# Kernel optimization log

Measured on AMD Instinct MI355X. Metric: run time of the kernel, lower is better.

Reference implementation:

```python
import jax, jax.numpy as jnp
import numpy as np
import math

WINDOW_LEFT = 512   # sliding-window: each query attends to keys in [q-512, q]
WINDOW_RIGHT = 0    # causal
NEG_INF = -1e30


def setup_inputs() -> dict:
    key = jax.random.key(0)
    kq, kk, kv, ks = jax.random.split(key, 4)
    B, S, H, D = 2, 2048, 16, 128
    q = jax.random.normal(kq, (B, S, H, D), dtype=jnp.float32)
    k = jax.random.normal(kk, (B, S, H, D), dtype=jnp.float32)
    v = jax.random.normal(kv, (B, S, H, D), dtype=jnp.float32)
    # geometric-ish ALiBi slopes per head (positive, decaying), like flash-attn
    alibi_slopes = jax.random.uniform(ks, (H,), dtype=jnp.float32, minval=0.001, maxval=0.5)
    return {"q": q, "k": k, "v": v, "alibi_slopes": alibi_slopes}


def reference(q, k, v, alibi_slopes):
    # q,k,v: [B, S, H, D]; alibi_slopes: [H]
    B, S, H, D = q.shape
    scale = 1.0 / math.sqrt(D)
    # scores: [B, H, Sq, Sk]
    scores = jnp.einsum("bqhd,bkhd->bhqk", q, k) * scale
    qi = jnp.arange(S)[:, None]
    ki = jnp.arange(S)[None, :]
    rel = ki - qi  # [Sq, Sk], <=0 for past keys
    # ALiBi bias (equal q/k lengths): -slope * |q - k|
    alibi = -alibi_slopes[:, None, None] * jnp.abs(rel).astype(scores.dtype)  # [H,Sq,Sk]
    scores = scores + alibi[None, :, :, :]
    # causal + sliding-window mask: allow WINDOW_RIGHT future, WINDOW_LEFT past
    mask = (rel <= WINDOW_RIGHT) & (rel >= -WINDOW_LEFT)  # [Sq, Sk]
    scores = jnp.where(mask[None, None, :, :], scores, NEG_INF)
    p = jax.nn.softmax(scores, axis=-1)
    out = jnp.einsum("bhqk,bkhd->bqhd", p, v)
    return out
```

## Files before the change

### kernel.cpp

```cpp
#include <hip/hip_runtime.h>
#include <hip/hip_bf16.h>

typedef __attribute__((ext_vector_type(8))) __bf16 bf16x8;
typedef __attribute__((ext_vector_type(2))) __bf16 bf16x2;
typedef __attribute__((ext_vector_type(4))) float f32x4;

#define MFMA32(a, b, c) __builtin_amdgcn_mfma_f32_16x16x32_bf16((a), (b), (c), 0, 0, 0)

constexpr int Bc = 2, Sc = 2048, Hc = 16, Dc = 128;
constexpr int HD = Hc * Dc;
constexpr int QB = 256;
constexpr float SCALE_L2 = (float)(0.08838834764831844 * 1.4426950408889634);
constexpr float LOG2E = 1.4426950408889634f;
constexpr float NEGF = -30000.0f;
constexpr int KSTR = 2080;

__device__ inline bf16x8 cvt8(f32x4 a, f32x4 b) {
    bf16x8 r;
    r[0]=(__bf16)a[0]; r[1]=(__bf16)a[1]; r[2]=(__bf16)a[2]; r[3]=(__bf16)a[3];
    r[4]=(__bf16)b[0]; r[5]=(__bf16)b[1]; r[6]=(__bf16)b[2]; r[7]=(__bf16)b[3];
    return r;
}

__global__ __launch_bounds__(512, 2) void lumen_attn_kernel(
    const float* __restrict__ Q, const float* __restrict__ K,
    const float* __restrict__ V, const float* __restrict__ SLP,
    float* __restrict__ O)
{
    __shared__ __align__(16) char k_lds[2][64 * 256];
    __shared__ __align__(16) char v_lds[2][8 * KSTR];

    const int tid  = threadIdx.x;
    const int lane = tid & 63;
    const int wid  = tid >> 6;
    const int cl = lane & 15;
    const int kg = lane >> 4;

    const int bid = blockIdx.x;
    const int swz = (bid & 7) * 32 + (bid >> 3);
    const int qb  = (swz & 7) * QB;
    const int bh  = swz >> 3;
    const int h = bh & 15, b = bh >> 4;

    const float slope = SLP[h] * LOG2E;
    const size_t base = (size_t)b * Sc * HD + (size_t)h * Dc;
    const float* qp = Q + base;
    const float* kp = K + base;
    const float* vp = V + base;
    float*       op = O + base;

    const int qw = qb + wid * 32;

    bf16x8 qf[2][4];
    #pragma unroll
    for (int s = 0; s < 2; ++s) {
        const float* qrow = qp + (size_t)(qw + s * 16 + cl) * HD + kg * 8;
        #pragma unroll
        for (int c = 0; c < 4; ++c) {
            f32x4 a = *(const f32x4*)(qrow + c * 32);
            f32x4 bq = *(const f32x4*)(qrow + c * 32 + 4);
            #pragma unroll
            for (int i = 0; i < 4; ++i) { a[i] *= SCALE_L2; bq[i] *= SCALE_L2; }
            qf[s][c] = cvt8(a, bq);
        }
    }

    f32x4 o_acc[2][8];
    #pragma unroll
    for (int s = 0; s < 2; ++s)
        #pragma unroll
        for (int nn = 0; nn < 8; ++nn) o_acc[s][nn] = f32x4{0.f, 0.f, 0.f, 0.f};
    float ssum[2] = {0.f, 0.f};

    int voff[8];
    #pragma unroll
    for (int nn = 0; nn < 8; ++nn) {
        const int d = nn * 16 + cl;
        const int s = (d & ~7) | ((d & 7) ^ ((d >> 3) & 7));
        voff[nn] = s * 16;
    }

    const int kb0    = qb > 512 ? qb - 512 : 0;
    const int kb_end = qb + QB - 64;
    const int NT     = (kb_end - kb0) / 64 + 1;

    const int ktk = tid >> 3;
    const int kd0 = (tid & 7) * 16;
    const int kpos = (2 * ((ktk >> 5) & 1) + ((ktk >> 2) & 1)) * 16
                   + ((ktk >> 3) & 3) * 4 + (ktk & 3);
    const int ksw = (kpos & 15) << 4;
    const int vtk = tid >> 4;
    const int vd0 = (tid & 15) * 8;
    const int va_ = tid & 15;

    f32x4 ra, rb, rc, rd, sa, sb, sc, sd;

    #define LOAD(kbn) do {                                                     \
        const float* kr_ = kp + (size_t)((kbn) + ktk) * HD + kd0;              \
        ra = *(const f32x4*)kr_;        rb = *(const f32x4*)(kr_ + 4);         \
        rc = *(const f32x4*)(kr_ + 8);  rd = *(const f32x4*)(kr_ + 12);        \
        const float* vr_ = vp + (size_t)((kbn) + 2 * vtk) * HD + vd0;          \
        sa = *(const f32x4*)vr_;        sb = *(const f32x4*)(vr_ + 4);         \
        sc = *(const f32x4*)(vr_ + HD); sd = *(const f32x4*)(vr_ + HD + 4);    \
    } while (0)

    #define WRITE(bi) do {                                                     \
        bf16x8 kw0_ = cvt8(ra, rb), kw1_ = cvt8(rc, rd);                       \
        char* kb_ = k_lds[bi] + kpos * 256;                                    \
        *(bf16x8*)(kb_ + ((kd0 * 2) ^ ksw))      = kw0_;                       \
        *(bf16x8*)(kb_ + ((kd0 * 2 + 16) ^ ksw)) = kw1_;                       \
        bf16x8 vw0_ = cvt8(sa, sb), vw1_ = cvt8(sc, sd);                       \
        char* vdst_ = v_lds[bi] + (vtk >> 2) * KSTR + (vtk & 3) * 4;           \
        _Pragma("unroll")                                                      \
        for (int j = 0; j < 8; ++j) {                                          \
            const int s_ = va_ * 8 + (j ^ (va_ & 7));                          \
            bf16x2 pk_; pk_[0] = vw0_[j]; pk_[1] = vw1_[j];                    \
            *(bf16x2*)(vdst_ + s_ * 16) = pk_;                                 \
        }                                                                      \
    } while (0)

    LOAD(kb0);
    WRITE(0);

    for (int i = 0; i < NT; ++i) {
        const int kb  = kb0 + i * 64;
        const int cur = i & 1;
        __syncthreads();

        if (i + 1 < NT) {
            LOAD(kb + 64);
            __builtin_amdgcn_sched_barrier(0);
        }

        if (!(kb > qw + 31 || kb + 63 < qw - 512)) {
            const char* kbuf = k_lds[cur];
            const char* vbuf = v_lds[cur];

            bf16x8 pa[2][2];
            #pragma unroll
            for (int n = 0; n < 4; ++n) {
                f32x4 s0 = f32x4{0.f, 0.f, 0.f, 0.f};
                f32x4 s1 = f32x4{0.f, 0.f, 0.f, 0.f};
                const char* kbse = kbuf + (n * 16 + cl) * 256;
                const int sw = cl << 4;
                #pragma unroll
                for (int c = 0; c < 4; ++c) {
                    bf16x8 kf = *(const bf16x8*)(kbse + (((c * 32 + kg * 8) * 2) ^ sw));
                    s0 = MFMA32(kf, qf[0][c], s0);
                    s1 = MFMA32(kf, qf[1][c], s1);
                }
                const int keyb = kb + kg * 8 + (n & 1) * 4 + ((n >> 1) << 5);
                #pragma unroll
                for (int s2 = 0; s2 < 2; ++s2) {
                    const f32x4 sv = s2 ? s1 : s0;
                    const int q = qw + s2 * 16 + cl;
                    #pragma unroll
                    for (int j = 0; j < 4; ++j) {
                        const int rel = q - (keyb + j);
                        const float val = ((unsigned)rel <= 512u)
                                          ? fmaf(-slope, (float)rel, sv[j]) : NEGF;
                        const float pe = exp2f(val);
                        ssum[s2] += pe;
                        pa[s2][n >> 1][(n & 1) * 4 + j] = (__bf16)pe;
                    }
                }
            }

            #pragma unroll
            for (int kk = 0; kk < 2; ++kk) {
                const char* vko = vbuf + (kk * 4 + kg) * KSTR;
                #pragma unroll
                for (int nn = 0; nn < 8; ++nn) {
                    bf16x8 vf = *(const bf16x8*)(vko + voff[nn]);
                    o_acc[0][nn] = MFMA32(pa[0][kk], vf, o_acc[0][nn]);
                    o_acc[1][nn] = MFMA32(pa[1][kk], vf, o_acc[1][nn]);
                }
            }
        }

        if (i + 1 < NT) {
            __builtin_amdgcn_sched_barrier(0);
            WRITE(cur ^ 1);
        }
    }

    const int r0 = kg << 2;
    #pragma unroll
    for (int s = 0; s < 2; ++s) {
        ssum[s] += __shfl_xor(ssum[s], 16);
        ssum[s] += __shfl_xor(ssum[s], 32);
    }
    #pragma unroll
    for (int s = 0; s < 2; ++s) {
        #pragma unroll
        for (int j = 0; j < 4; ++j) {
            const float sj = __shfl(ssum[s], r0 + j);
            const float inv = 1.0f / sj;
            float* orow = op + (size_t)(qw + s * 16 + r0 + j) * HD;
            #pragma unroll
            for (int nn = 0; nn < 8; ++nn)
                orow[nn * 16 + cl] = o_acc[s][nn][j] * inv;
        }
    }
    #undef LOAD
    #undef WRITE
}

extern "C" void kernel_launch(void* const* d_in, const int* in_sizes, int n_in,
                              void* d_out, int out_size, void* d_ws, size_t ws_size,
                              hipStream_t stream) {
    const float* q   = (const float*)d_in[0];
    const float* k   = (const float*)d_in[1];
    const float* v   = (const float*)d_in[2];
    const float* slp = (const float*)d_in[3];
    float* out = (float*)d_out;

    dim3 grid(Bc * Hc * (Sc / QB));
    lumen_attn_kernel<<<grid, dim3(512), 0, stream>>>(q, k, v, slp, out);
}
```

Baseline: 48.93 us.

## Compute softmax row sums via MFMA with ones and skip masking on interior tiles

Row sums of the exponentiated scores are now accumulated by multiplying the bf16 probability fragments against a ones vector with MFMA, rather than by scalar adds followed by cross-lane shuffles at the end. Tiles that lie fully inside the window get a fast path that drops the integer mask compare and select and computes the ALiBi offset in float. This trims VALU work in the softmax section and removes the final shuffle reduction. The cost is four extra MFMAs per tile, and the denominator is now summed from bf16-rounded values, so it matches the numerator but is less precise.

```diff
diff --git a/kernel.cpp b/kernel.cpp
--- a/kernel.cpp
+++ b/kernel.cpp
@@ -70,7 +70,13 @@
     for (int s = 0; s < 2; ++s)
         #pragma unroll
         for (int nn = 0; nn < 8; ++nn) o_acc[s][nn] = f32x4{0.f, 0.f, 0.f, 0.f};
-    float ssum[2] = {0.f, 0.f};
+    f32x4 ssacc[2];
+    ssacc[0] = f32x4{0.f, 0.f, 0.f, 0.f};
+    ssacc[1] = f32x4{0.f, 0.f, 0.f, 0.f};
+
+    bf16x8 ones8;
+    #pragma unroll
+    for (int i = 0; i < 8; ++i) ones8[i] = (__bf16)1.0f;
 
     int voff[8];
     #pragma unroll
@@ -135,6 +141,7 @@
         if (!(kb > qw + 31 || kb + 63 < qw - 512)) {
             const char* kbuf = k_lds[cur];
             const char* vbuf = v_lds[cur];
+            const bool interior = (kb <= qw - 63) && (kb >= qw - 481);
 
             bf16x8 pa[2][2];
             #pragma unroll
@@ -150,21 +157,39 @@
                     s1 = MFMA32(kf, qf[1][c], s1);
                 }
                 const int keyb = kb + kg * 8 + (n & 1) * 4 + ((n >> 1) << 5);
-                #pragma unroll
-                for (int s2 = 0; s2 < 2; ++s2) {
-                    const f32x4 sv = s2 ? s1 : s0;
-                    const int q = qw + s2 * 16 + cl;
+                if (interior) {
+                    const float f0 = (float)((qw + cl) - keyb);
                     #pragma unroll
-                    for (int j = 0; j < 4; ++j) {
-                        const int rel = q - (keyb + j);
-                        const float val = ((unsigned)rel <= 512u)
-                                          ? fmaf(-slope, (float)rel, sv[j]) : NEGF;
-                        const float pe = exp2f(val);
-                        ssum[s2] += pe;
-                        pa[s2][n >> 1][(n & 1) * 4 + j] = (__bf16)pe;
+                    for (int s2 = 0; s2 < 2; ++s2) {
+                        const f32x4 sv = s2 ? s1 : s0;
+                        const float fq = f0 + (float)(16 * s2);
+                        #pragma unroll
+                        for (int j = 0; j < 4; ++j) {
+                            const float pe = exp2f(fmaf(-slope, fq - (float)j, sv[j]));
+                            pa[s2][n >> 1][(n & 1) * 4 + j] = (__bf16)pe;
+                        }
+                    }
+                } else {
+                    #pragma unroll
+                    for (int s2 = 0; s2 < 2; ++s2) {
+                        const f32x4 sv = s2 ? s1 : s0;
+                        const int q = qw + s2 * 16 + cl;
+                        #pragma unroll
+                        for (int j = 0; j < 4; ++j) {
+                            const int rel = q - (keyb + j);
+                            const float val = ((unsigned)rel <= 512u)
+                                              ? fmaf(-slope, (float)rel, sv[j]) : NEGF;
+                            const float pe = exp2f(val);
+                            pa[s2][n >> 1][(n & 1) * 4 + j] = (__bf16)pe;
+                        }
                     }
                 }
             }
+
+            ssacc[0] = MFMA32(pa[0][0], ones8, ssacc[0]);
+            ssacc[0] = MFMA32(pa[0][1], ones8, ssacc[0]);
+            ssacc[1] = MFMA32(pa[1][0], ones8, ssacc[1]);
+            ssacc[1] = MFMA32(pa[1][1], ones8, ssacc[1]);
 
             #pragma unroll
             for (int kk = 0; kk < 2; ++kk) {
@@ -187,15 +212,9 @@
     const int r0 = kg << 2;
     #pragma unroll
     for (int s = 0; s < 2; ++s) {
-        ssum[s] += __shfl_xor(ssum[s], 16);
-        ssum[s] += __shfl_xor(ssum[s], 32);
-    }
-    #pragma unroll
-    for (int s = 0; s < 2; ++s) {
         #pragma unroll
         for (int j = 0; j < 4; ++j) {
-            const float sj = __shfl(ssum[s], r0 + j);
-            const float inv = 1.0f / sj;
+            const float inv = 1.0f / ssacc[s][j];
             float* orow = op + (size_t)(qw + s * 16 + r0 + j) * HD;
             #pragma unroll
             for (int nn = 0; nn < 8; ++nn)
```

Result: no change. 48.61 us (-0.6%).
